# Kernel tuning notes

Measured on AMD Instinct MI355X. Metric: run time of the kernel, lower is better.

Reference implementation:

```python
import jax, jax.numpy as jnp
import numpy as np

N = 16384
IN_DIM = 64
OUT_DIM = 64
BN_EPS = 1e-5
LEAKY_SLOPE = 0.01


def setup_inputs() -> dict:
    key = jax.random.key(0)
    k_g, k_h, k_w, k_b = jax.random.split(key, 4)
    g = jax.random.uniform(k_g, (N, N), dtype=jnp.float32)  # dense nonneg adjacency
    h = jax.random.normal(k_h, (N, IN_DIM), dtype=jnp.float32)
    W = jax.random.normal(k_w, (OUT_DIM, IN_DIM), dtype=jnp.float32) * (1.0 / np.sqrt(IN_DIM))
    b = jax.random.normal(k_b, (OUT_DIM,), dtype=jnp.float32) * 0.01
    gamma = jnp.ones((IN_DIM,), dtype=jnp.float32)
    beta = jnp.zeros((IN_DIM,), dtype=jnp.float32)
    return {"g": g, "h": h, "W": W, "b": b, "gamma": gamma, "beta": beta}


def reference(g, h, W, b, gamma, beta):
    # BatchNorm1d in training mode: batch statistics over the node axis
    mean = h.mean(axis=0)
    var = jnp.mean(jnp.square(h - mean), axis=0)  # biased variance, as torch BN
    hn = (h - mean) * (gamma / jnp.sqrt(var + BN_EPS)) + beta

    # g <- g + I  (add self-loops on the diagonal, no dense eye materialized)
    idx = jnp.arange(g.shape[0])
    ga = g.at[idx, idx].add(1.0)

    # D^{-1/2} A D^{-1/2}: torch builds diag matrices and does two N^3 matmuls;
    # mathematically identical row/column scaling (same values, O(N^2)).
    d_inv_sqrt = jax.lax.rsqrt(ga.sum(axis=1))  # [N]
    gn = ga * d_inv_sqrt[:, None] * d_inv_sqrt[None, :]

    # Linear projection, propagate, LeakyReLU
    hp = hn @ W.T + b                     # [N, out_dim]
    out = gn @ hp                         # [N, out_dim]
    return jnp.where(out >= 0, out, LEAKY_SLOPE * out)
```

## Files before the change

kernel.cpp:

```cpp
#include <hip/hip_runtime.h>
#include <hip/hip_bf16.h>

#define GN 16384
#define GDIM 64

typedef __attribute__((ext_vector_type(8))) short bf16x8;
typedef __attribute__((ext_vector_type(4))) float f32x4;

template <typename T>
__device__ __forceinline__ T ntl(const T* p) { return __builtin_nontemporal_load(p); }
template <typename T>
__device__ __forceinline__ void nts(T v, T* p) { __builtin_nontemporal_store(v, p); }

__device__ __forceinline__ unsigned short f2bf(float x) {
    unsigned int u = __builtin_bit_cast(unsigned int, x);
    u += 0x7fffu + ((u >> 16) & 1u);
    return (unsigned short)(u >> 16);
}

__device__ __forceinline__ short f2bf_hw(float x) {
    __hip_bfloat16 b = __float2bfloat16(x);
    return (short)__builtin_bit_cast(unsigned short, b);
}

__global__ void bn_partial(const float* __restrict__ h, float* __restrict__ ps,
                           float* __restrict__ pq) {
    int b = blockIdx.x, t = threadIdx.x;
    int col = t & 63, wr = t >> 6;
    float s = 0.f, q = 0.f;
    int base = b * 64;
    for (int rep = 0; rep < 16; ++rep) {
        int row = base + wr + rep * 4;
        float v = h[row * GDIM + col];
        s += v; q += v * v;
    }
    __shared__ float ls[4][64], lq[4][64];
    ls[wr][col] = s; lq[wr][col] = q;
    __syncthreads();
    if (t < 64) {
        ps[b * 64 + t] = ls[0][t] + ls[1][t] + ls[2][t] + ls[3][t];
        pq[b * 64 + t] = lq[0][t] + lq[1][t] + lq[2][t] + lq[3][t];
    }
}

__global__ void bn_finalize(const float* __restrict__ ps, const float* __restrict__ pq,
                            const float* __restrict__ W, const float* __restrict__ bvec,
                            const float* __restrict__ gamma, const float* __restrict__ beta,
                            float* __restrict__ Wp, float* __restrict__ bp) {
    int t = threadIdx.x;
    __shared__ float s_s[64], s_t2[64];
    if (t < 64) {
        float S = 0.f, Q = 0.f;
        for (int b = 0; b < 256; ++b) { S += ps[b * 64 + t]; Q += pq[b * 64 + t]; }
        float mean = S * (1.0f / 16384.0f);
        float var  = Q * (1.0f / 16384.0f) - mean * mean;
        float sc   = gamma[t] * rsqrtf(var + 1e-5f);
        s_s[t]  = sc;
        s_t2[t] = beta[t] - mean * sc;
    }
    __syncthreads();
    for (int k = 0; k < 16; ++k) {
        int idx = t + k * 256;
        Wp[idx] = s_s[idx & 63] * W[idx];
    }
    if (t < 64) {
        float acc = bvec[t];
        for (int c = 0; c < 64; ++c) acc += s_t2[c] * W[t * 64 + c];
        bp[t] = acc;
    }
}

__global__ void linear_hp(const float* __restrict__ h, const float* __restrict__ Wp,
                          const float* __restrict__ bpr, float* __restrict__ hp) {
    __shared__ float lw[64][65];
    __shared__ float lh[16][65];
    int t = threadIdx.x;
    int rb = blockIdx.x * 16;
    for (int k = 0; k < 16; ++k) {
        int idx = t + k * 256;
        lw[idx >> 6][idx & 63] = Wp[idx];
    }
    for (int k = 0; k < 4; ++k) {
        int idx = t + k * 256;
        lh[idx >> 6][idx & 63] = h[rb * GDIM + idx];
    }
    __syncthreads();
    int o = t & 63, rg = t >> 6;
    float a0 = 0.f, a1 = 0.f, a2 = 0.f, a3 = 0.f;
    for (int c = 0; c < 64; ++c) {
        float wv = lw[o][c];
        a0 += lh[rg][c]      * wv;
        a1 += lh[rg + 4][c]  * wv;
        a2 += lh[rg + 8][c]  * wv;
        a3 += lh[rg + 12][c] * wv;
    }
    float bb = bpr[o];
    hp[(rb + rg) * GDIM + o]      = a0 + bb;
    hp[(rb + rg + 4) * GDIM + o]  = a1 + bb;
    hp[(rb + rg + 8) * GDIM + o]  = a2 + bb;
    hp[(rb + rg + 12) * GDIM + o] = a3 + bb;
}

__global__ void rowsum_dinv(const float* __restrict__ g, float* __restrict__ dinv) {
    int row = blockIdx.x, t = threadIdx.x;
    const f32x4* grow = (const f32x4*)(g + (size_t)row * GN);
    float s = 0.f;
    for (int k = 0; k < 16; ++k) {
        f32x4 v = ntl(grow + t + k * 256);
        s += (v[0] + v[1]) + (v[2] + v[3]);
    }
    for (int off = 32; off; off >>= 1) s += __shfl_down(s, off, 64);
    __shared__ float wsum[4];
    if ((t & 63) == 0) wsum[t >> 6] = s;
    __syncthreads();
    if (t == 0) {
        float tot = (wsum[0] + wsum[1]) + (wsum[2] + wsum[3]) + 1.0f;
        dinv[row] = rsqrtf(tot);
    }
}

__global__ void make_hsT(const float* __restrict__ hp, const float* __restrict__ dinv,
                         unsigned short* __restrict__ hsT) {
    __shared__ float tile[64][65];
    int t = threadIdx.x;
    int jb = blockIdx.x * 64;
    int o = t & 63, jg = t >> 6;
    for (int k = 0; k < 16; ++k) {
        int j = jg + k * 4;
        tile[j][o] = hp[(jb + j) * GDIM + o] * dinv[jb + j];
    }
    __syncthreads();
    int oo = t >> 2, q = t & 3;
    for (int k = 0; k < 16; ++k) {
        int j = q * 16 + k;
        hsT[(size_t)oo * GN + jb + j] = f2bf(tile[j][oo]);
    }
}

__global__ void __launch_bounds__(256, 2) spmm_part(
    const float* __restrict__ g, const unsigned short* __restrict__ hsT,
    float* __restrict__ part)
{
    int t = threadIdx.x;
    int lane = t & 63;
    int w = t >> 6;
    int itile = blockIdx.x >> 2;
    int split = blockIdx.x & 3;
    int rb = itile * 64;
    int kb = split * 4096;
    int l15 = lane & 15;
    int kg = lane >> 4;

    f32x4 acc[4][4];
    #pragma unroll
    for (int m = 0; m < 4; ++m)
        #pragma unroll
        for (int n = 0; n < 4; ++n)
            #pragma unroll
            for (int r = 0; r < 4; ++r) acc[m][n][r] = 0.f;

    const float* abase = g + (size_t)(rb + l15) * GN + kb + kg * 8;
    const unsigned short* bbase = hsT + (size_t)l15 * GN + kb + kg * 8;

    int jo = w * 32;
    for (int it = 0; it < 32; ++it) {
        bf16x8 bfr[4];
        #pragma unroll
        for (int n = 0; n < 4; ++n)
            bfr[n] = *(const bf16x8*)(bbase + (size_t)n * 16 * GN + jo);
        #pragma unroll
        for (int m = 0; m < 4; ++m) {
            const float* ap = abase + (size_t)m * 16 * GN + jo;
            f32x4 x0 = ntl((const f32x4*)ap);
            f32x4 x1 = ntl((const f32x4*)ap + 1);
            bf16x8 afr;
            afr[0] = f2bf_hw(x0[0]); afr[1] = f2bf_hw(x0[1]);
            afr[2] = f2bf_hw(x0[2]); afr[3] = f2bf_hw(x0[3]);
            afr[4] = f2bf_hw(x1[0]); afr[5] = f2bf_hw(x1[1]);
            afr[6] = f2bf_hw(x1[2]); afr[7] = f2bf_hw(x1[3]);
            #pragma unroll
            for (int n = 0; n < 4; ++n)
                acc[m][n] = __builtin_amdgcn_mfma_f32_16x16x32_bf16(afr, bfr[n], acc[m][n], 0, 0, 0);
        }
        jo += 128;
    }

    __shared__ float red[64][64];
    if (w == 0) {
        #pragma unroll
        for (int m = 0; m < 4; ++m)
            #pragma unroll
            for (int n = 0; n < 4; ++n)
                #pragma unroll
                for (int r = 0; r < 4; ++r)
                    red[m * 16 + kg * 4 + r][n * 16 + l15] = acc[m][n][r];
    }
    __syncthreads();
    #pragma unroll
    for (int ww = 1; ww < 4; ++ww) {
        if (w == ww) {
            #pragma unroll
            for (int m = 0; m < 4; ++m)
                #pragma unroll
                for (int n = 0; n < 4; ++n)
                    #pragma unroll
                    for (int r = 0; r < 4; ++r)
                        red[m * 16 + kg * 4 + r][n * 16 + l15] += acc[m][n][r];
        }
        __syncthreads();
    }

    float* pdst = part + (size_t)split * (GN * GDIM) + (size_t)rb * GDIM;
    for (int kk = 0; kk < 4; ++kk) {
        int idx = t + kk * 256;
        f32x4 v;
        v[0] = red[(idx * 4) >> 6][(idx * 4) & 63];
        v[1] = red[(idx * 4 + 1) >> 6][(idx * 4 + 1) & 63];
        v[2] = red[(idx * 4 + 2) >> 6][(idx * 4 + 2) & 63];
        v[3] = red[(idx * 4 + 3) >> 6][(idx * 4 + 3) & 63];
        nts(v, (f32x4*)pdst + idx);
    }
}

__global__ void epilogue(const float* __restrict__ part, const float* __restrict__ hp,
                         const float* __restrict__ dinv, float* __restrict__ out) {
    int q = blockIdx.x * 256 + threadIdx.x;
    int i = q >> 4;
    int o = (q & 15) * 4;
    size_t off = (size_t)i * GDIM + o;
    const size_t S = (size_t)GN * GDIM;
    f32x4 s0 = ntl((const f32x4*)(part + off));
    f32x4 s1 = ntl((const f32x4*)(part + S + off));
    f32x4 s2 = ntl((const f32x4*)(part + 2 * S + off));
    f32x4 s3 = ntl((const f32x4*)(part + 3 * S + off));
    f32x4 hpv = *(const f32x4*)(hp + off);
    float di = dinv[i];
    f32x4 v = (s0 + s1) + (s2 + s3);
    #pragma unroll
    for (int r = 0; r < 4; ++r) {
        float x = di * (v[r] + di * hpv[r]);
        v[r] = (x >= 0.f) ? x : 0.01f * x;
    }
    nts(v, (f32x4*)(out + off));
}

extern "C" void kernel_launch(void* const* d_in, const int* in_sizes, int n_in,
                              void* d_out, int out_size, void* d_ws, size_t ws_size,
                              hipStream_t stream) {
    const float* g     = (const float*)d_in[0];
    const float* h     = (const float*)d_in[1];
    const float* W     = (const float*)d_in[2];
    const float* b     = (const float*)d_in[3];
    const float* gamma = (const float*)d_in[4];
    const float* beta  = (const float*)d_in[5];
    float* out = (float*)d_out;

    float* ws   = (float*)d_ws;
    float* ps   = ws;
    float* pq   = ws + 16384;
    float* Wp   = ws + 32768;
    float* bp   = ws + 36864;
    float* dinv = ws + 36928;
    float* hp   = ws + 53312;
    unsigned short* hsT = (unsigned short*)(ws + 1101888);
    float* part = ws + 1626176;

    bn_partial  <<<256,   256, 0, stream>>>(h, ps, pq);
    bn_finalize <<<1,     256, 0, stream>>>(ps, pq, W, b, gamma, beta, Wp, bp);
    linear_hp   <<<1024,  256, 0, stream>>>(h, Wp, bp, hp);
    rowsum_dinv <<<16384, 256, 0, stream>>>(g, dinv);
    make_hsT    <<<256,   256, 0, stream>>>(hp, dinv, hsT);
    spmm_part   <<<1024,  256, 0, stream>>>(g, hsT, part);
    epilogue    <<<1024,  256, 0, stream>>>(part, hp, dinv, out);
}
```

Before: 489.2 us.

## Restructure spmm to split rows across waves with LDS-staged shared B tiles

The propagation kernel now uses 512-thread blocks covering 256 rows. Each wave owns 32 distinct rows over the full K range, so the cross-wave LDS reduction is no longer needed. The bf16 hsT operand is staged into double-buffered LDS with global_load_lds and shared by all waves, replacing per-wave redundant global loads. This trades the reduction and repeated B fetches for a per-chunk barrier, a large LDS footprint (about 133 KB), and uncoalesced scalar output stores. The grid shrinks to 256 blocks, which may leave the GPU's compute units thinly occupied.

```diff
diff --git a/kernel.cpp b/kernel.cpp
--- a/kernel.cpp
+++ b/kernel.cpp
@@ -6,6 +6,9 @@
 
 typedef __attribute__((ext_vector_type(8))) short bf16x8;
 typedef __attribute__((ext_vector_type(4))) float f32x4;
+
+typedef __attribute__((address_space(1))) const void GASV;
+typedef __attribute__((address_space(3))) void LASV;
 
 template <typename T>
 __device__ __forceinline__ T ntl(const T* p) { return __builtin_nontemporal_load(p); }
@@ -137,89 +140,85 @@
     }
 }
 
-__global__ void __launch_bounds__(256, 2) spmm_part(
+__global__ void __launch_bounds__(512, 2) spmm_part(
     const float* __restrict__ g, const unsigned short* __restrict__ hsT,
     float* __restrict__ part)
 {
+    __shared__ unsigned short bs[2][64][520];
+
     int t = threadIdx.x;
     int lane = t & 63;
     int w = t >> 6;
     int itile = blockIdx.x >> 2;
     int split = blockIdx.x & 3;
-    int rb = itile * 64;
+    int rb = itile * 256;
     int kb = split * 4096;
     int l15 = lane & 15;
     int kg = lane >> 4;
 
-    f32x4 acc[4][4];
+    f32x4 acc[2][4];
     #pragma unroll
-    for (int m = 0; m < 4; ++m)
+    for (int m = 0; m < 2; ++m)
         #pragma unroll
         for (int n = 0; n < 4; ++n)
             #pragma unroll
             for (int r = 0; r < 4; ++r) acc[m][n][r] = 0.f;
 
-    const float* abase = g + (size_t)(rb + l15) * GN + kb + kg * 8;
-    const unsigned short* bbase = hsT + (size_t)l15 * GN + kb + kg * 8;
-
-    int jo = w * 32;
-    for (int it = 0; it < 32; ++it) {
-        bf16x8 bfr[4];
+    const float* abase = g + (size_t)(rb + w * 32 + l15) * GN + kb + kg * 8;
+
+    auto stage = [&](int kc, int buf) {
+        int ck = kb + kc * 512;
+        #pragma unroll
+        for (int q = 0; q < 8; ++q) {
+            int o = w * 8 + q;
+            const char* src = (const char*)(hsT + (size_t)o * GN + ck) + lane * 16;
+            __builtin_amdgcn_global_load_lds((GASV*)src, (LASV*)&bs[buf][o][0], 16, 0, 0);
+        }
+    };
+
+    stage(0, 0);
+    __syncthreads();
+
+    for (int c = 0; c < 8; ++c) {
+        int buf = c & 1;
+        if (c < 7) stage(c + 1, buf ^ 1);
+
+        int cbase = c * 512;
+        for (int it = 0; it < 16; ++it) {
+            int ko = it * 32 + kg * 8;
+            bf16x8 bfr[4];
+            #pragma unroll
+            for (int n = 0; n < 4; ++n)
+                bfr[n] = *(const bf16x8*)&bs[buf][n * 16 + l15][ko];
+            #pragma unroll
+            for (int m = 0; m < 2; ++m) {
+                const float* ap = abase + (size_t)m * 16 * GN + cbase + it * 32;
+                f32x4 x0 = ntl((const f32x4*)ap);
+                f32x4 x1 = ntl((const f32x4*)ap + 1);
+                bf16x8 afr;
+                afr[0] = f2bf_hw(x0[0]); afr[1] = f2bf_hw(x0[1]);
+                afr[2] = f2bf_hw(x0[2]); afr[3] = f2bf_hw(x0[3]);
+                afr[4] = f2bf_hw(x1[0]); afr[5] = f2bf_hw(x1[1]);
+                afr[6] = f2bf_hw(x1[2]); afr[7] = f2bf_hw(x1[3]);
+                #pragma unroll
+                for (int n = 0; n < 4; ++n)
+                    acc[m][n] = __builtin_amdgcn_mfma_f32_16x16x32_bf16(afr, bfr[n], acc[m][n], 0, 0, 0);
+            }
+        }
+        __syncthreads();
+    }
+
+    float* pdst = part + (size_t)split * (GN * GDIM);
+    #pragma unroll
+    for (int m = 0; m < 2; ++m)
         #pragma unroll
         for (int n = 0; n < 4; ++n)
-            bfr[n] = *(const bf16x8*)(bbase + (size_t)n * 16 * GN + jo);
-        #pragma unroll
-        for (int m = 0; m < 4; ++m) {
-            const float* ap = abase + (size_t)m * 16 * GN + jo;
-            f32x4 x0 = ntl((const f32x4*)ap);
-            f32x4 x1 = ntl((const f32x4*)ap + 1);
-            bf16x8 afr;
-            afr[0] = f2bf_hw(x0[0]); afr[1] = f2bf_hw(x0[1]);
-            afr[2] = f2bf_hw(x0[2]); afr[3] = f2bf_hw(x0[3]);
-            afr[4] = f2bf_hw(x1[0]); afr[5] = f2bf_hw(x1[1]);
-            afr[6] = f2bf_hw(x1[2]); afr[7] = f2bf_hw(x1[3]);
-            #pragma unroll
-            for (int n = 0; n < 4; ++n)
-                acc[m][n] = __builtin_amdgcn_mfma_f32_16x16x32_bf16(afr, bfr[n], acc[m][n], 0, 0, 0);
-        }
-        jo += 128;
-    }
-
-    __shared__ float red[64][64];
-    if (w == 0) {
-        #pragma unroll
-        for (int m = 0; m < 4; ++m)
-            #pragma unroll
-            for (int n = 0; n < 4; ++n)
-                #pragma unroll
-                for (int r = 0; r < 4; ++r)
-                    red[m * 16 + kg * 4 + r][n * 16 + l15] = acc[m][n][r];
-    }
-    __syncthreads();
-    #pragma unroll
-    for (int ww = 1; ww < 4; ++ww) {
-        if (w == ww) {
-            #pragma unroll
-            for (int m = 0; m < 4; ++m)
-                #pragma unroll
-                for (int n = 0; n < 4; ++n)
-                    #pragma unroll
-                    for (int r = 0; r < 4; ++r)
-                        red[m * 16 + kg * 4 + r][n * 16 + l15] += acc[m][n][r];
-        }
-        __syncthreads();
-    }
-
-    float* pdst = part + (size_t)split * (GN * GDIM) + (size_t)rb * GDIM;
-    for (int kk = 0; kk < 4; ++kk) {
-        int idx = t + kk * 256;
-        f32x4 v;
-        v[0] = red[(idx * 4) >> 6][(idx * 4) & 63];
-        v[1] = red[(idx * 4 + 1) >> 6][(idx * 4 + 1) & 63];
-        v[2] = red[(idx * 4 + 2) >> 6][(idx * 4 + 2) & 63];
-        v[3] = red[(idx * 4 + 3) >> 6][(idx * 4 + 3) & 63];
-        nts(v, (f32x4*)pdst + idx);
-    }
+            #pragma unroll
+            for (int r = 0; r < 4; ++r) {
+                int i = rb + w * 32 + m * 16 + kg * 4 + r;
+                int col = n * 16 + l15;
+                nts(acc[m][n][r], &pdst[(size_t)i * GDIM + col]);
+            }
 }
 
 __global__ void epilogue(const float* __restrict__ part, const float* __restrict__ hp,
@@ -270,6 +269,6 @@
     linear_hp   <<<1024,  256, 0, stream>>>(h, Wp, bp, hp);
     rowsum_dinv <<<16384, 256, 0, stream>>>(g, dinv);
     make_hsT    <<<256,   256, 0, stream>>>(hp, dinv, hsT);
-    spmm_part   <<<1024,  256, 0, stream>>>(g, hsT, part);
+    spmm_part   <<<256,   512, 0, stream>>>(g, hsT, part);
     epilogue    <<<1024,  256, 0, stream>>>(part, hp, dinv, out);
 }
```

New measurement: 454.4 us. 7.1% less time.
